# Kernel tuning notes

Hardware: AMD Instinct MI355X
Metric: run time of the kernel (lower is better)

## Reference

```python
import jax, jax.numpy as jnp
import numpy as np

N = 100000
D = 128
R = 4
E = 1600000
LN_EPS = 1e-3  # keras LayerNormalization default epsilon


def setup_inputs() -> dict:
    key = jax.random.key(0)
    ks = jax.random.split(key, 12)
    return {
        "node_embeddings": jax.random.normal(ks[0], (N, D), jnp.float32),
        "rel_embeddings": jax.random.normal(ks[1], (R, D), jnp.float32),
        "adj_rows": jax.random.randint(ks[2], (R, E), 0, N, jnp.int32),
        "adj_cols": jax.random.randint(ks[3], (R, E), 0, N, jnp.int32),
        "adj_vals": jax.random.uniform(ks[4], (R, E), jnp.float32),
        "W_fuse": jax.random.normal(ks[5], (2 * D, D), jnp.float32) * 0.05,
        "b_fuse": jnp.zeros((D,), jnp.float32),
        "W_rel": jax.random.normal(ks[6], (R, D, D), jnp.float32) * 0.05,
        "b_rel": jnp.zeros((R, D), jnp.float32),
        "rel_weights": jnp.ones((R,), jnp.float32),
        "W_gate": jax.random.normal(ks[7], (D, D), jnp.float32) * 0.05,
        "b_gate": jnp.zeros((D,), jnp.float32),
        "ln_gamma": jnp.ones((D,), jnp.float32),
        "ln_beta": jnp.zeros((D,), jnp.float32),
    }


def reference(node_embeddings, rel_embeddings, adj_rows, adj_cols, adj_vals,
              W_fuse, b_fuse, W_rel, b_rel, rel_weights, W_gate, b_gate,
              ln_gamma, ln_beta):
    n = node_embeddings.shape[0]
    rel_outs = []
    for r in range(R):  # small fixed relation count, structurally distinct kernels
        # sparse-dense matmul: messages[i] = sum_j A_r[i,j] * X[j]
        gathered = adj_vals[r][:, None] * node_embeddings[adj_cols[r]]  # [E, D]
        messages = jax.ops.segment_sum(gathered, adj_rows[r], num_segments=n)  # [N, D]
        rel_vec = jnp.broadcast_to(rel_embeddings[r], messages.shape)
        cat = jnp.concatenate([messages, rel_vec], axis=-1)  # [N, 2D]
        fused = jax.nn.relu(cat @ W_fuse + b_fuse)  # [N, D]
        rel_outs.append(fused @ W_rel[r] + b_rel[r])  # relation-specific kernel
    stacked = jnp.stack(rel_outs, axis=0)  # [R, N, D]
    w = jax.nn.softmax(rel_weights)
    combined = jnp.einsum('r,rnd->nd', w, stacked)
    gate = jax.nn.sigmoid(node_embeddings @ W_gate + b_gate)
    x = node_embeddings + gate * combined
    mu = jnp.mean(x, axis=-1, keepdims=True)
    var = jnp.mean((x - mu) ** 2, axis=-1, keepdims=True)
    out = (x - mu) * jax.lax.rsqrt(var + LN_EPS) * ln_gamma + ln_beta
    return out  # dropout is identity at inference (training=None)
```

## Files before the change

kernel.cpp:

```cpp
#include <hip/hip_runtime.h>
#include <math.h>

#define N_NODES 100000
#define DIM 128
#define NREL 4
#define NEDGE 1600000
#define LN_EPS 1e-3f

#define NBUCK 196
#define BCAP 10240
#define P1_VPT 16
#define P1_EDGES 4096

typedef __attribute__((ext_vector_type(8))) short bf16x8;
typedef __attribute__((ext_vector_type(4))) float f32x4;
typedef __attribute__((ext_vector_type(4))) unsigned int u32x4;

__device__ __forceinline__ float bf2f(unsigned short b) {
    return __uint_as_float(((unsigned int)b) << 16);
}
__device__ __forceinline__ unsigned short f2bf(float f) {
    unsigned int u = __float_as_uint(f);
    u += 0x7FFFu + ((u >> 16) & 1u);
    return (unsigned short)(u >> 16);
}

__global__ __launch_bounds__(512) void prep_kernel(
    const float* __restrict__ rel_emb, const float* __restrict__ W_fuse,
    const float* __restrict__ b_fuse, const float* __restrict__ rel_weights,
    float* __restrict__ bfr, float* __restrict__ wsm)
{
    int t = threadIdx.x;
    int r = t >> 7;
    int d = t & 127;
    float acc = b_fuse[d];
    for (int k = 0; k < DIM; ++k)
        acc += rel_emb[r * DIM + k] * W_fuse[(DIM + k) * DIM + d];
    bfr[r * DIM + d] = acc;
    if (t < NREL) {
        float m = rel_weights[0];
        for (int i = 1; i < NREL; ++i) m = fmaxf(m, rel_weights[i]);
        float s = 0.f;
        for (int i = 0; i < NREL; ++i) s += expf(rel_weights[i] - m);
        wsm[t] = expf(rel_weights[t] - m) / s;
    }
}

__global__ __launch_bounds__(256) void pack_kernel(
    const float* __restrict__ Wf, const float* __restrict__ Wr,
    const float* __restrict__ Wg,
    unsigned short* __restrict__ PH, unsigned short* __restrict__ PL)
{
    int mat = blockIdx.y;
    int idx = blockIdx.x * 256 + threadIdx.x;
    int j = idx & 7;
    int lane = (idx >> 3) & 63;
    int ntile = (idx >> 9) & 7;
    int kblk = idx >> 12;
    int k = kblk * 32 + (lane >> 4) * 8 + j;
    int n = ntile * 16 + (lane & 15);
    const float* src = (mat == 0) ? Wf :
                       (mat == 5) ? Wg : (Wr + (size_t)(mat - 1) * DIM * DIM);
    float w = src[k * DIM + n];
    unsigned short hi = f2bf(w);
    float lo = w - bf2f(hi);
    PH[mat * 16384 + idx] = hi;
    PL[mat * 16384 + idx] = f2bf(lo);
}

__global__ __launch_bounds__(256) void xb_kernel(
    const float* __restrict__ X, unsigned short* __restrict__ Xb)
{
    int idx = blockIdx.x * 256 + threadIdx.x;
    float4 f = ((const float4*)X)[idx];
    ushort4 o;
    o.x = f2bf(f.x); o.y = f2bf(f.y); o.z = f2bf(f.z); o.w = f2bf(f.w);
    ((ushort4*)Xb)[idx] = o;
}

__global__ __launch_bounds__(256) void y_kernel(
    const float* __restrict__ X,
    const unsigned short* __restrict__ PH,
    const unsigned short* __restrict__ PL,
    unsigned short* __restrict__ Yb)
{
    __shared__ unsigned short sXh[32 * 128];
    __shared__ unsigned short sXl[32 * 128];

    int t = threadIdx.x;
    int row0 = blockIdx.x * 32;
    int wv = t >> 6, l = t & 63, lq = l >> 4, lm = l & 15;

    const float4* Xs = (const float4*)(X + (size_t)row0 * DIM);
#pragma unroll
    for (int it = 0; it < 2; ++it) {
        int i = t + it * 256;
        float4 f0 = Xs[2 * i];
        float4 f1 = Xs[2 * i + 1];
        float e[8] = {f0.x, f0.y, f0.z, f0.w, f1.x, f1.y, f1.z, f1.w};
        unsigned short h[8], lo[8];
#pragma unroll
        for (int j = 0; j < 8; ++j) {
            h[j] = f2bf(e[j]);
            lo[j] = f2bf(e[j] - bf2f(h[j]));
        }
        uint4 hv, lv;
        hv.x = ((unsigned int)h[1] << 16) | h[0];
        hv.y = ((unsigned int)h[3] << 16) | h[2];
        hv.z = ((unsigned int)h[5] << 16) | h[4];
        hv.w = ((unsigned int)h[7] << 16) | h[6];
        lv.x = ((unsigned int)lo[1] << 16) | lo[0];
        lv.y = ((unsigned int)lo[3] << 16) | lo[2];
        lv.z = ((unsigned int)lo[5] << 16) | lo[4];
        lv.w = ((unsigned int)lo[7] << 16) | lo[6];
        int row = i >> 4, ck = i & 15;
        int off = row * 256 + ((ck * 16) ^ ((row & 7) << 4));
        *(uint4*)((char*)sXh + off) = hv;
        *(uint4*)((char*)sXl + off) = lv;
    }
    __syncthreads();

    f32x4 acc[2][2];
#pragma unroll
    for (int mt = 0; mt < 2; ++mt)
#pragma unroll
        for (int ni = 0; ni < 2; ++ni)
#pragma unroll
            for (int r = 0; r < 4; ++r) acc[mt][ni][r] = 0.f;

#pragma unroll
    for (int kb = 0; kb < 4; ++kb) {
        int c0 = kb * 64 + lq * 16;
        int r0 = lm, r1 = 16 + lm;
        int o0 = r0 * 256 + (c0 ^ ((r0 & 7) << 4));
        int o1 = r1 * 256 + (c0 ^ ((r1 & 7) << 4));
        bf16x8 ah0 = *(const bf16x8*)((char*)sXh + o0);
        bf16x8 ah1 = *(const bf16x8*)((char*)sXh + o1);
        bf16x8 al0 = *(const bf16x8*)((char*)sXl + o0);
        bf16x8 al1 = *(const bf16x8*)((char*)sXl + o1);
#pragma unroll
        for (int ni = 0; ni < 2; ++ni) {
            int nt_ = wv * 2 + ni;
            int fi = ((kb * 8 + nt_) * 64 + l) << 3;
            bf16x8 bh = *(const bf16x8*)(PH + fi);
            bf16x8 bl = *(const bf16x8*)(PL + fi);
            acc[0][ni] = __builtin_amdgcn_mfma_f32_16x16x32_bf16(ah0, bh, acc[0][ni], 0, 0, 0);
            acc[1][ni] = __builtin_amdgcn_mfma_f32_16x16x32_bf16(ah1, bh, acc[1][ni], 0, 0, 0);
            acc[0][ni] = __builtin_amdgcn_mfma_f32_16x16x32_bf16(ah0, bl, acc[0][ni], 0, 0, 0);
            acc[1][ni] = __builtin_amdgcn_mfma_f32_16x16x32_bf16(ah1, bl, acc[1][ni], 0, 0, 0);
            acc[0][ni] = __builtin_amdgcn_mfma_f32_16x16x32_bf16(al0, bh, acc[0][ni], 0, 0, 0);
            acc[1][ni] = __builtin_amdgcn_mfma_f32_16x16x32_bf16(al1, bh, acc[1][ni], 0, 0, 0);
        }
    }
    __syncthreads();
#pragma unroll
    for (int mt = 0; mt < 2; ++mt)
#pragma unroll
    for (int ni = 0; ni < 2; ++ni) {
        int colg = (wv * 2 + ni) * 16 + lm;
#pragma unroll
        for (int r = 0; r < 4; ++r) {
            int row = mt * 16 + lq * 4 + r;
            sXh[row * 128 + colg] = f2bf(acc[mt][ni][r]);
        }
    }
    __syncthreads();
    uint4* dst = (uint4*)(Yb + (size_t)row0 * DIM);
    const uint4* s4 = (const uint4*)sXh;
    dst[t] = s4[t];
    dst[t + 256] = s4[t + 256];
}

__global__ __launch_bounds__(256) void binA_kernel(
    const int* __restrict__ arows, const int* __restrict__ acols,
    const float* __restrict__ avals,
    int* __restrict__ bcnt,
    unsigned long long* __restrict__ edges2)
{
    __shared__ int hist[256];
    __shared__ int hoff[256];
    __shared__ int gbase[NBUCK];
    __shared__ unsigned long long stage[P1_EDGES];
    __shared__ unsigned short sbid[P1_EDGES];

    int t = threadIdx.x;
    int rl = blockIdx.y;
    int e0 = blockIdx.x * P1_EDGES;

    hist[t] = 0;
    __syncthreads();

    int b[P1_VPT], rank[P1_VPT], rloc[P1_VPT];
    unsigned int pay[P1_VPT];
#pragma unroll
    for (int i = 0; i < P1_VPT; ++i) {
        int e = e0 + i * 256 + t;
        b[i] = -1;
        if (e < NEDGE) {
            size_t off = (size_t)rl * NEDGE + e;
            int row = arows[off];
            unsigned int vb = __float_as_uint(avals[off]);
            vb += 0x7FFFu + ((vb >> 16) & 1u);
            pay[i] = ((unsigned int)acols[off] << 15) | ((vb >> 16) & 0x7FFFu);
            b[i] = row >> 9;
            rloc[i] = row & 511;
            rank[i] = atomicAdd(&hist[b[i]], 1);
        }
    }
    __syncthreads();

    int v = hist[t];
    int run = v;
    hoff[t] = run;
    __syncthreads();
    for (int o = 1; o < 256; o <<= 1) {
        int other = (t >= o) ? hoff[t - o] : 0;
        __syncthreads();
        run += other;
        hoff[t] = run;
        __syncthreads();
    }
    hoff[t] = run - v;
    if (t < NBUCK) {
        int g = (v > 0) ? atomicAdd(&bcnt[rl * NBUCK + t], v) : 0;
        gbase[t] = (rl * NBUCK + t) * BCAP + g;
    }
    __syncthreads();

#pragma unroll
    for (int i = 0; i < P1_VPT; ++i) {
        if (b[i] >= 0) {
            int slot = hoff[b[i]] + rank[i];
            stage[slot] = ((unsigned long long)rloc[i] << 32) | pay[i];
            sbid[slot] = (unsigned short)b[i];
        }
    }
    __syncthreads();

    int total = hoff[NBUCK - 1] + hist[NBUCK - 1];
    for (int idx = t; idx < total; idx += 256) {
        int bb = sbid[idx];
        int gaddr = gbase[bb] + (idx - hoff[bb]);
        if (gaddr - (rl * NBUCK + bb) * BCAP < BCAP)
            edges2[gaddr] = stage[idx];
    }
}

__global__ __launch_bounds__(1024) void bscan_kernel(
    const int* __restrict__ bcnt, int* __restrict__ bstart)
{
    __shared__ int s[1024];
    int t = threadIdx.x;
    int v = (t < NREL * NBUCK) ? min(bcnt[t], BCAP) : 0;
    int run = v;
    s[t] = run;
    __syncthreads();
    for (int o = 1; o < 1024; o <<= 1) {
        int other = (t >= o) ? s[t - o] : 0;
        __syncthreads();
        run += other;
        s[t] = run;
        __syncthreads();
    }
    if (t < NREL * NBUCK) bstart[t] = run - v;
}

__global__ __launch_bounds__(256) void binB_kernel(
    const unsigned long long* __restrict__ edges2,
    const int* __restrict__ bcnt, const int* __restrict__ bstart,
    int* __restrict__ rowstart, unsigned int* __restrict__ edges)
{
    __shared__ int rcnt[512];
    __shared__ int rpos[512];
    __shared__ int sc[256];

    int t = threadIdx.x;
    int b = blockIdx.x, rl = blockIdx.y;
    int gb = rl * NBUCK + b;
    int cnt = min(bcnt[gb], BCAP);
    const unsigned long long* src = edges2 + (size_t)gb * BCAP;
    int row0 = b << 9;
    int nrows = min(512, N_NODES - row0);

    rcnt[t] = 0; rcnt[t + 256] = 0;
    __syncthreads();
    for (int e = t; e < cnt; e += 256)
        atomicAdd(&rcnt[(int)(src[e] >> 32)], 1);
    __syncthreads();

    int v0 = rcnt[2 * t], v1 = rcnt[2 * t + 1];
    int tsum = v0 + v1;
    int run = tsum;
    sc[t] = run;
    __syncthreads();
    for (int o = 1; o < 256; o <<= 1) {
        int other = (t >= o) ? sc[t - o] : 0;
        __syncthreads();
        run += other;
        sc[t] = run;
        __syncthreads();
    }
    int base = bstart[gb];
    int excl = base + run - tsum;
    rpos[2 * t] = excl;
    rpos[2 * t + 1] = excl + v0;
    __syncthreads();

    for (int i = t; i < nrows; i += 256)
        rowstart[rl * N_NODES + row0 + i] = rpos[i];
    __syncthreads();

    for (int e = t; e < cnt; e += 256) {
        unsigned long long s = src[e];
        int p = atomicAdd(&rpos[(int)(s >> 32)], 1);
        edges[p] = (unsigned int)s;
    }
}

#define FMA8(acc, v, q)                                    \
    acc[0] += v * __uint_as_float((q).x << 16);            \
    acc[1] += v * __uint_as_float((q).x & 0xFFFF0000u);    \
    acc[2] += v * __uint_as_float((q).y << 16);            \
    acc[3] += v * __uint_as_float((q).y & 0xFFFF0000u);    \
    acc[4] += v * __uint_as_float((q).z << 16);            \
    acc[5] += v * __uint_as_float((q).z & 0xFFFF0000u);    \
    acc[6] += v * __uint_as_float((q).w << 16);            \
    acc[7] += v * __uint_as_float((q).w & 0xFFFF0000u);

__global__ __launch_bounds__(256) void gather_kernel(
    const unsigned short* __restrict__ Yb,
    const int* __restrict__ rowstart,
    const unsigned int* __restrict__ edges,
    const float* __restrict__ bfr,
    unsigned short* __restrict__ msgs)
{
    int t = threadIdx.x;
    int grp = t >> 4, lane = t & 15;
    int row = blockIdx.x * 16 + grp;
    int rl = blockIdx.y;
    int g = rl * N_NODES + row;
    int s = rowstart[g];
    int e = (g == NREL * N_NODES - 1) ? (NREL * NEDGE) : rowstart[g + 1];

    float a0[8], a1[8], a2[8], a3[8];
#pragma unroll
    for (int i = 0; i < 8; ++i) { a0[i] = 0.f; a1[i] = 0.f; a2[i] = 0.f; a3[i] = 0.f; }

    const uint4* Yb4 = (const uint4*)Yb;
    int ee = s;
    int nrem = e - s;
    if (nrem >= 4) {
        unsigned int p0 = __builtin_nontemporal_load(edges + ee);
        unsigned int p1 = __builtin_nontemporal_load(edges + ee + 1);
        unsigned int p2 = __builtin_nontemporal_load(edges + ee + 2);
        unsigned int p3 = __builtin_nontemporal_load(edges + ee + 3);
        while (nrem >= 4) {
            uint4 q0 = Yb4[((size_t)(p0 >> 15) << 4) + lane];
            uint4 q1 = Yb4[((size_t)(p1 >> 15) << 4) + lane];
            uint4 q2 = Yb4[((size_t)(p2 >> 15) << 4) + lane];
            uint4 q3 = Yb4[((size_t)(p3 >> 15) << 4) + lane];
            float v0 = __uint_as_float((p0 & 0x7FFFu) << 16);
            float v1 = __uint_as_float((p1 & 0x7FFFu) << 16);
            float v2 = __uint_as_float((p2 & 0x7FFFu) << 16);
            float v3 = __uint_as_float((p3 & 0x7FFFu) << 16);
            nrem -= 4; ee += 4;
            if (nrem >= 4) {
                p0 = __builtin_nontemporal_load(edges + ee);
                p1 = __builtin_nontemporal_load(edges + ee + 1);
                p2 = __builtin_nontemporal_load(edges + ee + 2);
                p3 = __builtin_nontemporal_load(edges + ee + 3);
            }
            FMA8(a0, v0, q0)
            FMA8(a1, v1, q1)
            FMA8(a2, v2, q2)
            FMA8(a3, v3, q3)
        }
    }
    while (nrem > 0) {
        unsigned int p = __builtin_nontemporal_load(edges + ee);
        uint4 q = Yb4[((size_t)(p >> 15) << 4) + lane];
        float v = __uint_as_float((p & 0x7FFFu) << 16);
        FMA8(a0, v, q)
        ++ee; --nrem;
    }
#pragma unroll
    for (int i = 0; i < 8; ++i) a0[i] += a1[i] + a2[i] + a3[i];

    const float4* bb = (const float4*)(bfr + rl * DIM + lane * 8);
    float4 b0 = bb[0], b1 = bb[1];
    float f0 = fmaxf(a0[0] + b0.x, 0.f), f1 = fmaxf(a0[1] + b0.y, 0.f);
    float f2 = fmaxf(a0[2] + b0.z, 0.f), f3 = fmaxf(a0[3] + b0.w, 0.f);
    float f4 = fmaxf(a0[4] + b1.x, 0.f), f5 = fmaxf(a0[5] + b1.y, 0.f);
    float f6 = fmaxf(a0[6] + b1.z, 0.f), f7 = fmaxf(a0[7] + b1.w, 0.f);
    u32x4 o;
    o[0] = ((unsigned int)f2bf(f1) << 16) | f2bf(f0);
    o[1] = ((unsigned int)f2bf(f3) << 16) | f2bf(f2);
    o[2] = ((unsigned int)f2bf(f5) << 16) | f2bf(f4);
    o[3] = ((unsigned int)f2bf(f7) << 16) | f2bf(f6);
    __builtin_nontemporal_store(o, (u32x4*)(msgs + ((size_t)g << 7)) + lane);
}

__global__ __launch_bounds__(256) void gemm2_kernel(
    const unsigned short* __restrict__ msgs,
    const float* __restrict__ X,
    const unsigned short* __restrict__ PH,
    const unsigned short* __restrict__ PL,
    const float* __restrict__ br,
    const float* __restrict__ wsm,
    const float* __restrict__ bg,
    const float* __restrict__ gamma,
    const float* __restrict__ beta,
    float* __restrict__ out)
{
    __shared__ float sX[32 * 132];
    __shared__ float red[32][8], red2[32][8];
    __shared__ float smu[32], srs[32];
    unsigned short* sB = (unsigned short*)sX;

    int t = threadIdx.x;
    int row0 = blockIdx.x * 32;
    int wv = t >> 6, l = t & 63, lq = l >> 4, lm = l & 15;

    f32x4 comb[2][2];
#pragma unroll
    for (int mt = 0; mt < 2; ++mt)
#pragma unroll
        for (int ni = 0; ni < 2; ++ni)
#pragma unroll
            for (int r = 0; r < 4; ++r) comb[mt][ni][r] = 0.f;

    uint4 m0, m1;
    {
        const uint4* src = (const uint4*)msgs + ((size_t)row0 << 4);
        m0 = src[t]; m1 = src[t + 256];
    }
    float4 xa, xb_, xc, xd;

    for (int rl = 0; rl < NREL; ++rl) {
        __syncthreads();
        {
            int i0 = t, i1 = t + 256;
            int row = i0 >> 4, ck = i0 & 15;
            *(uint4*)((char*)sB + row * 256 + ((ck * 16) ^ ((row & 7) << 4))) = m0;
            row = i1 >> 4; ck = i1 & 15;
            *(uint4*)((char*)sB + row * 256 + ((ck * 16) ^ ((row & 7) << 4))) = m1;
        }
        if (rl < NREL - 1) {
            const uint4* src = (const uint4*)msgs +
                ((size_t)((rl + 1) * N_NODES + row0) << 4);
            m0 = src[t]; m1 = src[t + 256];
        } else {
            const float4* Xs = (const float4*)(X + (size_t)row0 * DIM);
            xa = Xs[2 * t];       xb_ = Xs[2 * t + 1];
            xc = Xs[2 * (t + 256)]; xd = Xs[2 * (t + 256) + 1];
        }
        __syncthreads();

        const unsigned short* ph2 = PH + (size_t)(1 + rl) * 16384;
        const unsigned short* pl2 = PL + (size_t)(1 + rl) * 16384;
        f32x4 acc[2][2];
#pragma unroll
        for (int mt = 0; mt < 2; ++mt)
#pragma unroll
            for (int ni = 0; ni < 2; ++ni)
#pragma unroll
                for (int r = 0; r < 4; ++r) acc[mt][ni][r] = 0.f;

#pragma unroll
        for (int kb = 0; kb < 4; ++kb) {
            int c0 = kb * 64 + lq * 16;
            int r0 = lm, r1 = 16 + lm;
            int o0 = r0 * 256 + (c0 ^ ((r0 & 7) << 4));
            int o1 = r1 * 256 + (c0 ^ ((r1 & 7) << 4));
            bf16x8 a0v = *(const bf16x8*)((char*)sB + o0);
            bf16x8 a1v = *(const bf16x8*)((char*)sB + o1);
#pragma unroll
            for (int ni = 0; ni < 2; ++ni) {
                int nt_ = wv * 2 + ni;
                int fi = ((kb * 8 + nt_) * 64 + l) << 3;
                bf16x8 bh = *(const bf16x8*)(ph2 + fi);
                bf16x8 bl = *(const bf16x8*)(pl2 + fi);
                acc[0][ni] = __builtin_amdgcn_mfma_f32_16x16x32_bf16(a0v, bh, acc[0][ni], 0, 0, 0);
                acc[1][ni] = __builtin_amdgcn_mfma_f32_16x16x32_bf16(a1v, bh, acc[1][ni], 0, 0, 0);
                acc[0][ni] = __builtin_amdgcn_mfma_f32_16x16x32_bf16(a0v, bl, acc[0][ni], 0, 0, 0);
                acc[1][ni] = __builtin_amdgcn_mfma_f32_16x16x32_bf16(a1v, bl, acc[1][ni], 0, 0, 0);
            }
        }
        {
            float wr_ = wsm[rl];
#pragma unroll
            for (int mt = 0; mt < 2; ++mt)
#pragma unroll
            for (int ni = 0; ni < 2; ++ni) {
                int colg = (wv * 2 + ni) * 16 + lm;
                float b = br[rl * DIM + colg];
#pragma unroll
                for (int r = 0; r < 4; ++r)
                    comb[mt][ni][r] += wr_ * (acc[mt][ni][r] + b);
            }
        }
    }

    __syncthreads();
    {
        float e0[8] = {xa.x, xa.y, xa.z, xa.w, xb_.x, xb_.y, xb_.z, xb_.w};
        uint4 hv;
        hv.x = ((unsigned int)f2bf(e0[1]) << 16) | f2bf(e0[0]);
        hv.y = ((unsigned int)f2bf(e0[3]) << 16) | f2bf(e0[2]);
        hv.z = ((unsigned int)f2bf(e0[5]) << 16) | f2bf(e0[4]);
        hv.w = ((unsigned int)f2bf(e0[7]) << 16) | f2bf(e0[6]);
        int i = t, row = i >> 4, ck = i & 15;
        *(uint4*)((char*)sB + row * 256 + ((ck * 16) ^ ((row & 7) << 4))) = hv;
        float e1[8] = {xc.x, xc.y, xc.z, xc.w, xd.x, xd.y, xd.z, xd.w};
        hv.x = ((unsigned int)f2bf(e1[1]) << 16) | f2bf(e1[0]);
        hv.y = ((unsigned int)f2bf(e1[3]) << 16) | f2bf(e1[2]);
        hv.z = ((unsigned int)f2bf(e1[5]) << 16) | f2bf(e1[4]);
        hv.w = ((unsigned int)f2bf(e1[7]) << 16) | f2bf(e1[6]);
        i = t + 256; row = i >> 4; ck = i & 15;
        *(uint4*)((char*)sB + row * 256 + ((ck * 16) ^ ((row & 7) << 4))) = hv;
    }
    __syncthreads();

    f32x4 accg[2][2];
#pragma unroll
    for (int mt = 0; mt < 2; ++mt)
#pragma unroll
        for (int ni = 0; ni < 2; ++ni)
#pragma unroll
            for (int r = 0; r < 4; ++r) accg[mt][ni][r] = 0.f;

    const unsigned short* phg = PH + (size_t)5 * 16384;
    const unsigned short* plg = PL + (size_t)5 * 16384;
#pragma unroll
    for (int kb = 0; kb < 4; ++kb) {
        int c0 = kb * 64 + lq * 16;
        int r0 = lm, r1 = 16 + lm;
        bf16x8 a0v = *(const bf16x8*)((char*)sB + r0 * 256 + (c0 ^ ((r0 & 7) << 4)));
        bf16x8 a1v = *(const bf16x8*)((char*)sB + r1 * 256 + (c0 ^ ((r1 & 7) << 4)));
#pragma unroll
        for (int ni = 0; ni < 2; ++ni) {
            int nt_ = wv * 2 + ni;
            int fi = ((kb * 8 + nt_) * 64 + l) << 3;
            bf16x8 bh = *(const bf16x8*)(phg + fi);
            bf16x8 bl = *(const bf16x8*)(plg + fi);
            accg[0][ni] = __builtin_amdgcn_mfma_f32_16x16x32_bf16(a0v, bh, accg[0][ni], 0, 0, 0);
            accg[1][ni] = __builtin_amdgcn_mfma_f32_16x16x32_bf16(a1v, bh, accg[1][ni], 0, 0, 0);
            accg[0][ni] = __builtin_amdgcn_mfma_f32_16x16x32_bf16(a0v, bl, accg[0][ni], 0, 0, 0);
            accg[1][ni] = __builtin_amdgcn_mfma_f32_16x16x32_bf16(a1v, bl, accg[1][ni], 0, 0, 0);
        }
    }
    __syncthreads();

#pragma unroll
    for (int mt = 0; mt < 2; ++mt)
#pragma unroll
    for (int ni = 0; ni < 2; ++ni) {
        int colg = (wv * 2 + ni) * 16 + lm;
        float bgv = bg[colg];
#pragma unroll
        for (int r = 0; r < 4; ++r) {
            int row = mt * 16 + lq * 4 + r;
            float g = 1.f / (1.f + expf(-(accg[mt][ni][r] + bgv)));
            float xv = X[(size_t)(row0 + row) * DIM + colg] + g * comb[mt][ni][r];
            sX[row * 132 + colg] = xv;
        }
    }
    __syncthreads();

    {
        int row = t >> 3, seg = t & 7;
        float s = 0.f, s2 = 0.f;
#pragma unroll
        for (int i = 0; i < 16; ++i) {
            float v = sX[row * 132 + seg * 16 + i];
            s += v; s2 += v * v;
        }
        red[row][seg] = s;
        red2[row][seg] = s2;
    }
    __syncthreads();
    if ((t & 7) == 0) {
        int row = t >> 3;
        float ts = 0.f, ts2 = 0.f;
#pragma unroll
        for (int i = 0; i < 8; ++i) { ts += red[row][i]; ts2 += red2[row][i]; }
        float mu = ts / DIM;
        float var = ts2 / DIM - mu * mu;
        smu[row] = mu;
        srs[row] = rsqrtf(var + LN_EPS);
    }
    __syncthreads();
    {
        float gm0 = gamma[l], gm1 = gamma[l + 64];
        float bt0 = beta[l],  bt1 = beta[l + 64];
#pragma unroll
        for (int rr = 0; rr < 8; ++rr) {
            int row = wv * 8 + rr;
            size_t gi = (size_t)(row0 + row) * DIM + l;
            out[gi]      = (sX[row * 132 + l]      - smu[row]) * srs[row] * gm0 + bt0;
            out[gi + 64] = (sX[row * 132 + l + 64] - smu[row]) * srs[row] * gm1 + bt1;
        }
    }
}

__global__ __launch_bounds__(256) void hist_kernel(
    const int* __restrict__ arows, int* __restrict__ counts)
{
    int e = blockIdx.x * 256 + threadIdx.x;
    int rl = blockIdx.y;
    if (e < NEDGE) {
        int row = arows[(size_t)rl * NEDGE + e];
        atomicAdd(&counts[rl * N_NODES + row], 1);
    }
}

__global__ __launch_bounds__(256) void scan1_kernel(
    int* __restrict__ counts, int* __restrict__ chunksums, int M)
{
    __shared__ int s[256];
    int chunk = blockIdx.x, t = threadIdx.x;
    int base = chunk * 1024 + t * 4;
    int v0 = (base + 0 < M) ? counts[base + 0] : 0;
    int v1 = (base + 1 < M) ? counts[base + 1] : 0;
    int v2 = (base + 2 < M) ? counts[base + 2] : 0;
    int v3 = (base + 3 < M) ? counts[base + 3] : 0;
    int p1 = v0, p2 = v0 + v1, p3 = v0 + v1 + v2, tsum = p3 + v3;
    int run = tsum;
    s[t] = run;
    __syncthreads();
    for (int off = 1; off < 256; off <<= 1) {
        int other = (t >= off) ? s[t - off] : 0;
        __syncthreads();
        run += other;
        s[t] = run;
        __syncthreads();
    }
    int excl = run - tsum;
    if (t == 255) chunksums[chunk] = run;
    if (base + 0 < M) counts[base + 0] = excl;
    if (base + 1 < M) counts[base + 1] = excl + p1;
    if (base + 2 < M) counts[base + 2] = excl + p2;
    if (base + 3 < M) counts[base + 3] = excl + p3;
}

__global__ __launch_bounds__(512) void scan2_kernel(
    int* __restrict__ chunksums, int nchunks)
{
    __shared__ int s[512];
    int t = threadIdx.x;
    int v = (t < nchunks) ? chunksums[t] : 0;
    int run = v;
    s[t] = run;
    __syncthreads();
    for (int off = 1; off < 512; off <<= 1) {
        int other = (t >= off) ? s[t - off] : 0;
        __syncthreads();
        run += other;
        s[t] = run;
        __syncthreads();
    }
    if (t < nchunks) chunksums[t] = run - v;
}

__global__ __launch_bounds__(256) void reorder_kernel(
    const int* __restrict__ arows, const int* __restrict__ acols,
    const float* __restrict__ avals,
    int* __restrict__ counts, const int* __restrict__ chunks,
    unsigned int* __restrict__ edges)
{
    int e = blockIdx.x * 256 + threadIdx.x;
    int rl = blockIdx.y;
    if (e < NEDGE) {
        size_t off = (size_t)rl * NEDGE + e;
        int row = arows[off];
        int g = rl * N_NODES + row;
        int pos = atomicAdd(&counts[g], 1) + chunks[g >> 10];
        unsigned int vb = __float_as_uint(avals[off]);
        vb += 0x7FFFu + ((vb >> 16) & 1u);
        edges[pos] = ((unsigned int)acols[off] << 15) | ((vb >> 16) & 0x7FFFu);
    }
}

__global__ __launch_bounds__(256) void mega_kernel(
    const unsigned short* __restrict__ Xb,
    const float* __restrict__ X,
    const int* __restrict__ counts,
    const int* __restrict__ chunks,
    const unsigned int* __restrict__ edges,
    const float* __restrict__ W1,
    const float* __restrict__ bfr,
    const float* __restrict__ Wr,
    const float* __restrict__ br,
    const float* __restrict__ wsm,
    const float* __restrict__ Wg,
    const float* __restrict__ bg,
    const float* __restrict__ gamma,
    const float* __restrict__ beta,
    float* __restrict__ out)
{
    __shared__ float sIn[32][DIM];
    __shared__ float red[32][8], red2[32][8];
    __shared__ float smu[32], srs[32];

    int t = threadIdx.x;
    int row0 = blockIdx.x * 32;
    int w = t >> 6;
    int l = t & 63;
    int grp = t >> 5, lane = t & 31;

    float comb_acc[8][2];
#pragma unroll
    for (int rr = 0; rr < 8; ++rr) { comb_acc[rr][0] = 0.f; comb_acc[rr][1] = 0.f; }

    for (int rl = 0; rl < NREL; ++rl) {
        __syncthreads();
#pragma unroll
        for (int i = 0; i < 4; ++i) {
            int ln = grp * 4 + i;
            int g = rl * N_NODES + row0 + ln;
            int s = (g == 0) ? 0 : counts[g - 1] + chunks[(g - 1) >> 10];
            int e = counts[g] + chunks[g >> 10];
            float4 a0 = make_float4(0.f, 0.f, 0.f, 0.f);
            int ee = s;
            for (; ee < e; ++ee) {
                unsigned int p0 = edges[ee];
                const ushort4* x0 = (const ushort4*)(Xb + ((size_t)(p0 >> 15) << 7));
                ushort4 q0 = x0[lane];
                float v0 = __uint_as_float((p0 & 0x7FFFu) << 16);
                a0.x += v0 * bf2f(q0.x); a0.y += v0 * bf2f(q0.y);
                a0.z += v0 * bf2f(q0.z); a0.w += v0 * bf2f(q0.w);
            }
            ((float4*)&sIn[ln][0])[lane] = a0;
        }
        __syncthreads();

        float acc1[8][2];
#pragma unroll
        for (int rr = 0; rr < 8; ++rr) { acc1[rr][0] = 0.f; acc1[rr][1] = 0.f; }
        for (int k4 = 0; k4 < DIM / 4; ++k4) {
            float wa[4], wb4[4];
#pragma unroll
            for (int j = 0; j < 4; ++j) {
                wa[j]  = W1[(k4 * 4 + j) * DIM + l];
                wb4[j] = W1[(k4 * 4 + j) * DIM + l + 64];
            }
#pragma unroll
            for (int rr = 0; rr < 8; ++rr) {
                float4 m = *(const float4*)&sIn[w * 8 + rr][k4 * 4];
                acc1[rr][0] += m.x * wa[0]  + m.y * wa[1]  + m.z * wa[2]  + m.w * wa[3];
                acc1[rr][1] += m.x * wb4[0] + m.y * wb4[1] + m.z * wb4[2] + m.w * wb4[3];
            }
        }
        __syncthreads();
        {
            float b0 = bfr[rl * DIM + l], b1 = bfr[rl * DIM + l + 64];
#pragma unroll
            for (int rr = 0; rr < 8; ++rr) {
                sIn[w * 8 + rr][l]      = fmaxf(acc1[rr][0] + b0, 0.f);
                sIn[w * 8 + rr][l + 64] = fmaxf(acc1[rr][1] + b1, 0.f);
            }
        }
        __syncthreads();

        const float* W2 = Wr + (size_t)rl * DIM * DIM;
        float acc2[8][2];
#pragma unroll
        for (int rr = 0; rr < 8; ++rr) { acc2[rr][0] = 0.f; acc2[rr][1] = 0.f; }
        for (int k4 = 0; k4 < DIM / 4; ++k4) {
            float wa[4], wb4[4];
#pragma unroll
            for (int j = 0; j < 4; ++j) {
                wa[j]  = W2[(k4 * 4 + j) * DIM + l];
                wb4[j] = W2[(k4 * 4 + j) * DIM + l + 64];
            }
#pragma unroll
            for (int rr = 0; rr < 8; ++rr) {
                float4 m = *(const float4*)&sIn[w * 8 + rr][k4 * 4];
                acc2[rr][0] += m.x * wa[0]  + m.y * wa[1]  + m.z * wa[2]  + m.w * wa[3];
                acc2[rr][1] += m.x * wb4[0] + m.y * wb4[1] + m.z * wb4[2] + m.w * wb4[3];
            }
        }
        {
            float wr_ = wsm[rl];
            float bb0 = br[rl * DIM + l], bb1 = br[rl * DIM + l + 64];
#pragma unroll
            for (int rr = 0; rr < 8; ++rr) {
                comb_acc[rr][0] += wr_ * (acc2[rr][0] + bb0);
                comb_acc[rr][1] += wr_ * (acc2[rr][1] + bb1);
            }
        }
    }

    __syncthreads();
    {
        const float4* src = (const float4*)(X + (size_t)row0 * DIM);
        float4* dst = (float4*)&sIn[0][0];
        for (int i = t; i < 32 * DIM / 4; i += 256) dst[i] = src[i];
    }
    __syncthreads();

    float accg[8][2];
#pragma unroll
    for (int rr = 0; rr < 8; ++rr) { accg[rr][0] = 0.f; accg[rr][1] = 0.f; }
    for (int k4 = 0; k4 < DIM / 4; ++k4) {
        float wa[4], wb4[4];
#pragma unroll
        for (int j = 0; j < 4; ++j) {
            wa[j]  = Wg[(k4 * 4 + j) * DIM + l];
            wb4[j] = Wg[(k4 * 4 + j) * DIM + l + 64];
        }
#pragma unroll
        for (int rr = 0; rr < 8; ++rr) {
            float4 m = *(const float4*)&sIn[w * 8 + rr][k4 * 4];
            accg[rr][0] += m.x * wa[0]  + m.y * wa[1]  + m.z * wa[2]  + m.w * wa[3];
            accg[rr][1] += m.x * wb4[0] + m.y * wb4[1] + m.z * wb4[2] + m.w * wb4[3];
        }
    }
    float xv[8][2];
    {
        float bg0 = bg[l], bg1 = bg[l + 64];
#pragma unroll
        for (int rr = 0; rr < 8; ++rr) {
            int row = w * 8 + rr;
            float g0 = 1.f / (1.f + expf(-(accg[rr][0] + bg0)));
            float g1 = 1.f / (1.f + expf(-(accg[rr][1] + bg1)));
            xv[rr][0] = sIn[row][l]      + g0 * comb_acc[rr][0];
            xv[rr][1] = sIn[row][l + 64] + g1 * comb_acc[rr][1];
        }
    }
    __syncthreads();
#pragma unroll
    for (int rr = 0; rr < 8; ++rr) {
        sIn[w * 8 + rr][l]      = xv[rr][0];
        sIn[w * 8 + rr][l + 64] = xv[rr][1];
    }
    __syncthreads();

    {
        int row = t >> 3, seg = t & 7;
        float s = 0.f, s2 = 0.f;
#pragma unroll
        for (int i = 0; i < 16; ++i) {
            float v = sIn[row][seg * 16 + i];
            s += v; s2 += v * v;
        }
        red[row][seg] = s;
        red2[row][seg] = s2;
    }
    __syncthreads();
    if ((t & 7) == 0) {
        int row = t >> 3;
        float ts = 0.f, ts2 = 0.f;
#pragma unroll
        for (int i = 0; i < 8; ++i) { ts += red[row][i]; ts2 += red2[row][i]; }
        float mu = ts / DIM;
        float var = ts2 / DIM - mu * mu;
        smu[row] = mu;
        srs[row] = rsqrtf(var + LN_EPS);
    }
    __syncthreads();
    {
        float gm0 = gamma[l], gm1 = gamma[l + 64];
        float bt0 = beta[l],  bt1 = beta[l + 64];
#pragma unroll
        for (int rr = 0; rr < 8; ++rr) {
            int row = w * 8 + rr;
            size_t gi = (size_t)(row0 + row) * DIM + l;
            out[gi]      = (sIn[row][l]      - smu[row]) * srs[row] * gm0 + bt0;
            out[gi + 64] = (sIn[row][l + 64] - smu[row]) * srs[row] * gm1 + bt1;
        }
    }
}

extern "C" void kernel_launch(void* const* d_in, const int* in_sizes, int n_in,
                              void* d_out, int out_size, void* d_ws, size_t ws_size,
                              hipStream_t stream) {
    const float* X     = (const float*)d_in[0];
    const float* rel   = (const float*)d_in[1];
    const int*   arows = (const int*)d_in[2];
    const int*   acols = (const int*)d_in[3];
    const float* avals = (const float*)d_in[4];
    const float* Wf    = (const float*)d_in[5];
    const float* bf    = (const float*)d_in[6];
    const float* Wr    = (const float*)d_in[7];
    const float* br    = (const float*)d_in[8];
    const float* rw    = (const float*)d_in[9];
    const float* Wg    = (const float*)d_in[10];
    const float* bg    = (const float*)d_in[11];
    const float* gamma = (const float*)d_in[12];
    const float* beta  = (const float*)d_in[13];
    float* out = (float*)d_out;

    const size_t XB_B = (size_t)N_NODES * DIM * 2;
    const size_t ED_B = (size_t)NREL * NEDGE * 4;
    const size_t CT_B = (size_t)NREL * N_NODES * 4;
    char* p = (char*)d_ws;
    unsigned short* Yb     = (unsigned short*)p;  p += XB_B;
    unsigned int*   edges  = (unsigned int*)p;    p += ED_B;
    int*            counts = (int*)p;             p += CT_B;
    int*            chunks = (int*)p;             p += 512 * 4;
    float*          bfr    = (float*)p;           p += NREL * DIM * 4;
    float*          wsm    = (float*)p;           p += 64 * 4;
    int*            bcnt   = (int*)p;             p += NREL * NBUCK * 4;
    int*            bstart = (int*)p;             p += (NREL * NBUCK + 1) * 4;
    unsigned short* PH     = (unsigned short*)p;  p += 6 * 16384 * 2;
    unsigned short* PL     = (unsigned short*)p;  p += 6 * 16384 * 2;
    size_t off = (size_t)(p - (char*)d_ws);
    off = (off + 255) & ~(size_t)255;
    unsigned short* msgs = (unsigned short*)((char*)d_ws + off);
    unsigned long long* edges2 = (unsigned long long*)msgs;
    const size_t need = off + (size_t)NREL * N_NODES * DIM * 2;
    const bool split = (ws_size >= need);

    prep_kernel<<<1, 512, 0, stream>>>(rel, Wf, bf, rw, bfr, wsm);
    pack_kernel<<<dim3(64, 6), 256, 0, stream>>>(Wf, Wr, Wg, PH, PL);

    if (split) {
        y_kernel<<<N_NODES / 32, 256, 0, stream>>>(X, PH, PL, Yb);
        hipMemsetAsync(bcnt, 0, (size_t)NREL * NBUCK * sizeof(int), stream);
        const int AB = (NEDGE + P1_EDGES - 1) / P1_EDGES;
        binA_kernel<<<dim3(AB, NREL), 256, 0, stream>>>(
            arows, acols, avals, bcnt, edges2);
        bscan_kernel<<<1, 1024, 0, stream>>>(bcnt, bstart);
        binB_kernel<<<dim3(NBUCK, NREL), 256, 0, stream>>>(
            edges2, bcnt, bstart, counts, edges);
        gather_kernel<<<dim3(N_NODES / 16, NREL), 256, 0, stream>>>(
            Yb, counts, edges, bfr, msgs);
        gemm2_kernel<<<N_NODES / 32, 256, 0, stream>>>(
            msgs, X, PH, PL, br, wsm, bg, gamma, beta, out);
    } else {
        xb_kernel<<<N_NODES * DIM / 4 / 256, 256, 0, stream>>>(X, Yb);
        const int EB = (NEDGE + 255) / 256;
        const int M = NREL * N_NODES;
        const int nch = (M + 1023) / 1024;
        hipMemsetAsync(counts, 0, (size_t)M * sizeof(int), stream);
        hist_kernel<<<dim3(EB, NREL), 256, 0, stream>>>(arows, counts);
        scan1_kernel<<<nch, 256, 0, stream>>>(counts, chunks, M);
        scan2_kernel<<<1, 512, 0, stream>>>(chunks, nch);
        reorder_kernel<<<dim3(EB, NREL), 256, 0, stream>>>(
            arows, acols, avals, counts, chunks, edges);
        mega_kernel<<<N_NODES / 32, 256, 0, stream>>>(
            Yb, X, counts, chunks, edges, Wf, bfr, Wr, br, wsm,
            Wg, bg, gamma, beta, out);
    }
}
```

Baseline: 637.0 us.

## Split Y into column halves so gather uses a half-size row working set

The y_kernel now writes the bf16 projected node table as two column-half planes, each 64 columns wide. The gather kernel is launched over (node block, relation×half), with 8 lanes per row, so each pass gathers from a 12.8MB half-table that fits better in cache. The cost is that the edge lists are read twice. Nontemporal loads and stores are replaced with plain ones. gemm2 now reuses X values already loaded in registers (xa..xd) by staging them in shared memory, instead of re-reading X from global memory in the epilogue.

New measurement: 598.1 us. 6.1% less time.

```diff
diff --git a/kernel.cpp b/kernel.cpp
--- a/kernel.cpp
+++ b/kernel.cpp
@@ -14,7 +14,6 @@
 
 typedef __attribute__((ext_vector_type(8))) short bf16x8;
 typedef __attribute__((ext_vector_type(4))) float f32x4;
-typedef __attribute__((ext_vector_type(4))) unsigned int u32x4;
 
 __device__ __forceinline__ float bf2f(unsigned short b) {
     return __uint_as_float(((unsigned int)b) << 16);
@@ -165,10 +164,16 @@
         }
     }
     __syncthreads();
-    uint4* dst = (uint4*)(Yb + (size_t)row0 * DIM);
     const uint4* s4 = (const uint4*)sXh;
-    dst[t] = s4[t];
-    dst[t + 256] = s4[t + 256];
+#pragma unroll
+    for (int it = 0; it < 2; ++it) {
+        int i = t + it * 256;
+        int row = i >> 4, ck = i & 15;
+        int half = ck >> 3, c64 = ck & 7;
+        uint4* dst = (uint4*)(Yb + (size_t)half * N_NODES * 64 +
+                              (size_t)(row0 + row) * 64);
+        dst[c64] = s4[i];
+    }
 }
 
 __global__ __launch_bounds__(256) void binA_kernel(
@@ -335,9 +340,10 @@
     unsigned short* __restrict__ msgs)
 {
     int t = threadIdx.x;
-    int grp = t >> 4, lane = t & 15;
-    int row = blockIdx.x * 16 + grp;
-    int rl = blockIdx.y;
+    int grp = t >> 3, lane = t & 7;
+    int row = blockIdx.x * 32 + grp;
+    int rl = blockIdx.y & 3;
+    int h  = blockIdx.y >> 2;
     int g = rl * N_NODES + row;
     int s = rowstart[g];
     int e = (g == NREL * N_NODES - 1) ? (NREL * NEDGE) : rowstart[g + 1];
@@ -346,29 +352,25 @@
 #pragma unroll
     for (int i = 0; i < 8; ++i) { a0[i] = 0.f; a1[i] = 0.f; a2[i] = 0.f; a3[i] = 0.f; }
 
-    const uint4* Yb4 = (const uint4*)Yb;
+    const uint4* Yb4 = (const uint4*)(Yb + (size_t)h * N_NODES * 64);
     int ee = s;
     int nrem = e - s;
     if (nrem >= 4) {
-        unsigned int p0 = __builtin_nontemporal_load(edges + ee);
-        unsigned int p1 = __builtin_nontemporal_load(edges + ee + 1);
-        unsigned int p2 = __builtin_nontemporal_load(edges + ee + 2);
-        unsigned int p3 = __builtin_nontemporal_load(edges + ee + 3);
+        unsigned int p0 = edges[ee], p1 = edges[ee + 1],
+                     p2 = edges[ee + 2], p3 = edges[ee + 3];
         while (nrem >= 4) {
-            uint4 q0 = Yb4[((size_t)(p0 >> 15) << 4) + lane];
-            uint4 q1 = Yb4[((size_t)(p1 >> 15) << 4) + lane];
-            uint4 q2 = Yb4[((size_t)(p2 >> 15) << 4) + lane];
-            uint4 q3 = Yb4[((size_t)(p3 >> 15) << 4) + lane];
+            uint4 q0 = Yb4[((size_t)(p0 >> 15) << 3) + lane];
+            uint4 q1 = Yb4[((size_t)(p1 >> 15) << 3) + lane];
+            uint4 q2 = Yb4[((size_t)(p2 >> 15) << 3) + lane];
+            uint4 q3 = Yb4[((size_t)(p3 >> 15) << 3) + lane];
             float v0 = __uint_as_float((p0 & 0x7FFFu) << 16);
             float v1 = __uint_as_float((p1 & 0x7FFFu) << 16);
             float v2 = __uint_as_float((p2 & 0x7FFFu) << 16);
             float v3 = __uint_as_float((p3 & 0x7FFFu) << 16);
             nrem -= 4; ee += 4;
             if (nrem >= 4) {
-                p0 = __builtin_nontemporal_load(edges + ee);
-                p1 = __builtin_nontemporal_load(edges + ee + 1);
-                p2 = __builtin_nontemporal_load(edges + ee + 2);
-                p3 = __builtin_nontemporal_load(edges + ee + 3);
+                p0 = edges[ee + 0]; p1 = edges[ee + 1];
+                p2 = edges[ee + 2]; p3 = edges[ee + 3];
             }
             FMA8(a0, v0, q0)
             FMA8(a1, v1, q1)
@@ -377,8 +379,8 @@
         }
     }
     while (nrem > 0) {
-        unsigned int p = __builtin_nontemporal_load(edges + ee);
-        uint4 q = Yb4[((size_t)(p >> 15) << 4) + lane];
+        unsigned int p = edges[ee];
+        uint4 q = Yb4[((size_t)(p >> 15) << 3) + lane];
         float v = __uint_as_float((p & 0x7FFFu) << 16);
         FMA8(a0, v, q)
         ++ee; --nrem;
@@ -386,18 +388,18 @@
 #pragma unroll
     for (int i = 0; i < 8; ++i) a0[i] += a1[i] + a2[i] + a3[i];
 
-    const float4* bb = (const float4*)(bfr + rl * DIM + lane * 8);
+    const float4* bb = (const float4*)(bfr + rl * DIM + h * 64 + lane * 8);
     float4 b0 = bb[0], b1 = bb[1];
     float f0 = fmaxf(a0[0] + b0.x, 0.f), f1 = fmaxf(a0[1] + b0.y, 0.f);
     float f2 = fmaxf(a0[2] + b0.z, 0.f), f3 = fmaxf(a0[3] + b0.w, 0.f);
     float f4 = fmaxf(a0[4] + b1.x, 0.f), f5 = fmaxf(a0[5] + b1.y, 0.f);
     float f6 = fmaxf(a0[6] + b1.z, 0.f), f7 = fmaxf(a0[7] + b1.w, 0.f);
-    u32x4 o;
-    o[0] = ((unsigned int)f2bf(f1) << 16) | f2bf(f0);
-    o[1] = ((unsigned int)f2bf(f3) << 16) | f2bf(f2);
-    o[2] = ((unsigned int)f2bf(f5) << 16) | f2bf(f4);
-    o[3] = ((unsigned int)f2bf(f7) << 16) | f2bf(f6);
-    __builtin_nontemporal_store(o, (u32x4*)(msgs + ((size_t)g << 7)) + lane);
+    uint4 o;
+    o.x = ((unsigned int)f2bf(f1) << 16) | f2bf(f0);
+    o.y = ((unsigned int)f2bf(f3) << 16) | f2bf(f2);
+    o.z = ((unsigned int)f2bf(f5) << 16) | f2bf(f4);
+    o.w = ((unsigned int)f2bf(f7) << 16) | f2bf(f6);
+    ((uint4*)(msgs + ((size_t)g << 7) + h * 64))[lane] = o;
 }
 
 __global__ __launch_bounds__(256) void gemm2_kernel(
@@ -551,6 +553,16 @@
     }
     __syncthreads();
 
+    {
+        int i = t, row = i >> 4, c = (i & 15) << 3;
+        *(float4*)&sX[row * 132 + c] = xa;
+        *(float4*)&sX[row * 132 + c + 4] = xb_;
+        i = t + 256; row = i >> 4; c = (i & 15) << 3;
+        *(float4*)&sX[row * 132 + c] = xc;
+        *(float4*)&sX[row * 132 + c + 4] = xd;
+    }
+    __syncthreads();
+
 #pragma unroll
     for (int mt = 0; mt < 2; ++mt)
 #pragma unroll
@@ -561,8 +573,7 @@
         for (int r = 0; r < 4; ++r) {
             int row = mt * 16 + lq * 4 + r;
             float g = 1.f / (1.f + expf(-(accg[mt][ni][r] + bgv)));
-            float xv = X[(size_t)(row0 + row) * DIM + colg] + g * comb[mt][ni][r];
-            sX[row * 132 + colg] = xv;
+            sX[row * 132 + colg] += g * comb[mt][ni][r];
         }
     }
     __syncthreads();
@@ -924,7 +935,7 @@
         bscan_kernel<<<1, 1024, 0, stream>>>(bcnt, bstart);
         binB_kernel<<<dim3(NBUCK, NREL), 256, 0, stream>>>(
             edges2, bcnt, bstart, counts, edges);
-        gather_kernel<<<dim3(N_NODES / 16, NREL), 256, 0, stream>>>(
+        gather_kernel<<<dim3(N_NODES / 32, NREL * 2), 256, 0, stream>>>(
             Yb, counts, edges, bfr, msgs);
         gemm2_kernel<<<N_NODES / 32, 256, 0, stream>>>(
             msgs, X, PH, PL, br, wsm, bg, gamma, beta, out);
```
